# Performance work log

Hardware: AMD Instinct MI355X
Metric: run time of the kernel (lower is better)

Reference implementation:

```python
import jax, jax.numpy as jnp
import numpy as np

NUM_GROUPS = 32
NUM_HEADS = 4
EPS = 1e-5


def setup_inputs() -> dict:
    key = jax.random.key(0)
    ks = jax.random.split(key, 6)
    B, C, H, W = 16, 512, 32, 32
    x = jax.random.normal(ks[0], (B, C, H, W), dtype=jnp.float32)
    gn_w = jax.random.normal(ks[1], (C,), dtype=jnp.float32) * 0.02 + 1.0
    gn_b = jax.random.normal(ks[2], (C,), dtype=jnp.float32) * 0.02
    # 1x1 convs are channel matmuls: store as [out_ch, in_ch]
    w_qkv = jax.random.normal(ks[3], (3 * C, C), dtype=jnp.float32) * (C ** -0.5)
    w_out = jax.random.normal(ks[4], (C, C), dtype=jnp.float32) * (C ** -0.5)
    b_out = jax.random.normal(ks[5], (C,), dtype=jnp.float32) * 0.02
    return {"x": x, "gn_w": gn_w, "gn_b": gn_b, "w_qkv": w_qkv, "w_out": w_out, "b_out": b_out}


def _group_norm(x, w, b):
    B, C, H, W = x.shape
    g = NUM_GROUPS
    xg = x.reshape(B, g, C // g, H, W)
    mean = xg.mean(axis=(2, 3, 4), keepdims=True)
    var = xg.var(axis=(2, 3, 4), keepdims=True)
    xn = ((xg - mean) * jax.lax.rsqrt(var + EPS)).reshape(B, C, H, W)
    return xn * w[None, :, None, None] + b[None, :, None, None]


def reference(x, gn_w, gn_b, w_qkv, w_out, b_out):
    B, C, H, W = x.shape
    h = NUM_HEADS
    d = C // h
    scale = d ** -0.5
    xn = _group_norm(x, gn_w, gn_b)
    # 1x1 conv QKV projection: [3C, C] @ channels
    qkv = jnp.einsum('oc,bchw->bohw', w_qkv, xn)
    q, k, v = jnp.split(qkv, 3, axis=1)
    # [B, h, d, HW]
    q = q.reshape(B, h, d, H * W)
    k = k.reshape(B, h, d, H * W)
    v = v.reshape(B, h, d, H * W)
    scores = jnp.einsum('bhdi,bhdj->bhij', q, k) * scale
    probs = jax.nn.softmax(scores, axis=-1)
    out = jnp.einsum('bhij,bhdj->bhdi', probs, v)
    out = out.reshape(B, C, H, W)
    out = jnp.einsum('oc,bchw->bohw', w_out, out) + b_out[None, :, None, None]
    return out + x
```

## Files before the change

kernel.cpp:

```cpp
#include <hip/hip_runtime.h>
#include <hip/hip_bf16.h>

#define B_    16
#define C_    512
#define HW_   1024
#define G_    32
#define CPG_  16
#define NH_   4
#define D_    128
#define EPS_  1e-5f
#define SCALE_ 0.08838834764831845f
#define SCALE_L2E_ 0.1275174306f

typedef short bf16x8 __attribute__((ext_vector_type(8)));
typedef short bf16x4 __attribute__((ext_vector_type(4)));
typedef float f32x4  __attribute__((ext_vector_type(4)));
typedef float f32x16 __attribute__((ext_vector_type(16)));

typedef __attribute__((address_space(3))) unsigned int lds_u32_t;
typedef const __attribute__((address_space(1))) unsigned int glb_u32_t;

__device__ __forceinline__ bf16x8 ld8(const __hip_bfloat16* p) {
    return *reinterpret_cast<const bf16x8*>(p);
}
__device__ __forceinline__ void gload16(const __hip_bfloat16* g, __hip_bfloat16* l) {
    __builtin_amdgcn_global_load_lds((glb_u32_t*)(const void*)g,
                                     (lds_u32_t*)(void*)l, 16, 0, 0);
}
__device__ __forceinline__ unsigned cvtpk_bf16(float lo, float hi) {
    unsigned r;
    asm("v_cvt_pk_bf16_f32 %0, %1, %2" : "=v"(r) : "v"(lo), "v"(hi));
    return r;
}

__global__ __launch_bounds__(256) void convert_w(
    const float* __restrict__ wqkv, const float* __restrict__ wout,
    __hip_bfloat16* __restrict__ wqkv_bf, __hip_bfloat16* __restrict__ wout_bf) {
    const int i = (blockIdx.x * 256 + threadIdx.x) * 4;
    if (i < 3 * C_ * C_) {
        float4 v = *reinterpret_cast<const float4*>(wqkv + i);
        union { bf16x4 s; __hip_bfloat16 h[4]; } u;
        u.h[0] = __float2bfloat16(v.x); u.h[1] = __float2bfloat16(v.y);
        u.h[2] = __float2bfloat16(v.z); u.h[3] = __float2bfloat16(v.w);
        *reinterpret_cast<bf16x4*>(wqkv_bf + i) = u.s;
    }
    if (i < C_ * C_) {
        float4 v = *reinterpret_cast<const float4*>(wout + i);
        union { bf16x4 s; __hip_bfloat16 h[4]; } u;
        u.h[0] = __float2bfloat16(v.x); u.h[1] = __float2bfloat16(v.y);
        u.h[2] = __float2bfloat16(v.z); u.h[3] = __float2bfloat16(v.w);
        *reinterpret_cast<bf16x4*>(wout_bf + i) = u.s;
    }
}

__global__ __launch_bounds__(256) void gn_kernel(
    const float* __restrict__ x, const float* __restrict__ gnw,
    const float* __restrict__ gnb, __hip_bfloat16* __restrict__ xn_t) {
    const int b = blockIdx.x >> 5;
    const int g = blockIdx.x & 31;
    const float* xp = x + ((size_t)(b * C_ + g * CPG_)) * HW_;

    float s = 0.f, s2 = 0.f;
    const float4* xv = reinterpret_cast<const float4*>(xp);
    #pragma unroll
    for (int t = 0; t < 16; ++t) {
        float4 v = xv[threadIdx.x + t * 256];
        s  += v.x + v.y + v.z + v.w;
        s2 += v.x * v.x + v.y * v.y + v.z * v.z + v.w * v.w;
    }
    #pragma unroll
    for (int off = 32; off > 0; off >>= 1) {
        s  += __shfl_down(s,  off, 64);
        s2 += __shfl_down(s2, off, 64);
    }
    __shared__ float ss[4], ss2[4];
    if ((threadIdx.x & 63) == 0) { ss[threadIdx.x >> 6] = s; ss2[threadIdx.x >> 6] = s2; }
    __syncthreads();
    s = ss[0] + ss[1] + ss[2] + ss[3];
    s2 = ss2[0] + ss2[1] + ss2[2] + ss2[3];
    const float mean = s * (1.f / 16384.f);
    const float inv  = rsqrtf(fmaxf(s2 * (1.f / 16384.f) - mean * mean, 0.f) + EPS_);

    float a[16], bb[16];
    #pragma unroll
    for (int cc = 0; cc < 16; ++cc) {
        float w = gnw[g * CPG_ + cc];
        a[cc] = inv * w;
        bb[cc] = gnb[g * CPG_ + cc] - mean * inv * w;
    }

    for (int hw = threadIdx.x; hw < HW_; hw += 256) {
        union { bf16x8 v; __hip_bfloat16 h[8]; } u0, u1;
        #pragma unroll
        for (int cc = 0; cc < 8; ++cc)
            u0.h[cc] = __float2bfloat16(xp[cc * HW_ + hw] * a[cc] + bb[cc]);
        #pragma unroll
        for (int cc = 8; cc < 16; ++cc)
            u1.h[cc - 8] = __float2bfloat16(xp[cc * HW_ + hw] * a[cc] + bb[cc]);
        __hip_bfloat16* dst = xn_t + ((size_t)(b * HW_ + hw)) * C_ + g * CPG_;
        *reinterpret_cast<bf16x8*>(dst) = u0.v;
        *reinterpret_cast<bf16x8*>(dst + 8) = u1.v;
    }
}

#define PH_(r, s) (((r) * 8 + ((s) ^ ((r) & 7))) * 8)

__global__ __launch_bounds__(256, 2) void qkv_gemm(
    const __hip_bfloat16* __restrict__ W, const __hip_bfloat16* __restrict__ xn_t,
    __hip_bfloat16* __restrict__ q_t, __hip_bfloat16* __restrict__ k_t,
    __hip_bfloat16* __restrict__ v_s) {
    const int id   = blockIdx.x;
    const int virt = (id & 7) * 192 + (id >> 3);
    const int ot   = virt % 12;
    const int rest = virt / 12;
    const int itl  = rest & 7;
    const int b    = rest >> 3;
    const int o0 = ot * 128, i0 = itl * 128;

    const int t = threadIdx.x;
    const int w = t >> 6, lane = t & 63, l16 = lane & 15, lg = lane >> 4;
    const int wr = w >> 1, wc = w & 1;
    const __hip_bfloat16* xb = xn_t + (size_t)b * HW_ * C_;

    __shared__ __align__(16) __hip_bfloat16 Ab[2][128 * 64];
    __shared__ __align__(16) __hip_bfloat16 Bb[2][128 * 64];

    const int r8  = lane >> 3;
    const int ssl = (lane & 7) ^ r8;
    auto issue = [&](int kk, int bi) {
        #pragma unroll
        for (int j = 0; j < 4; ++j) {
            const int row = w * 32 + j * 8 + r8;
            gload16(W  + (size_t)(o0 + row) * C_ + kk + ssl * 8, &Ab[bi][(w * 32 + j * 8) * 64]);
            gload16(xb + (size_t)(i0 + row) * C_ + kk + ssl * 8, &Bb[bi][(w * 32 + j * 8) * 64]);
        }
    };

    f32x4 acc[4][4];
    const f32x4 z = {0.f, 0.f, 0.f, 0.f};
    #pragma unroll
    for (int m = 0; m < 4; ++m)
        #pragma unroll
        for (int n = 0; n < 4; ++n) acc[m][n] = z;

    issue(0, 0);
    for (int ks = 0; ks < 8; ++ks) {
        __syncthreads();
        if (ks < 7) issue((ks + 1) * 64, (ks + 1) & 1);
        const __hip_bfloat16* Ac = Ab[ks & 1];
        const __hip_bfloat16* Bc = Bb[ks & 1];
        #pragma unroll
        for (int kks = 0; kks < 2; ++kks) {
            bf16x8 af[4], bfr[4];
            #pragma unroll
            for (int m = 0; m < 4; ++m)
                af[m] = ld8(&Ac[PH_(wr * 64 + m * 16 + l16, kks * 4 + lg)]);
            #pragma unroll
            for (int n = 0; n < 4; ++n)
                bfr[n] = ld8(&Bc[PH_(wc * 64 + n * 16 + l16, kks * 4 + lg)]);
            if (ot < 8) {
                #pragma unroll
                for (int m = 0; m < 4; ++m)
                    #pragma unroll
                    for (int n = 0; n < 4; ++n)
                        acc[m][n] = __builtin_amdgcn_mfma_f32_16x16x32_bf16(bfr[n], af[m], acc[m][n], 0, 0, 0);
            } else {
                #pragma unroll
                for (int m = 0; m < 4; ++m)
                    #pragma unroll
                    for (int n = 0; n < 4; ++n)
                        acc[m][n] = __builtin_amdgcn_mfma_f32_16x16x32_bf16(af[m], bfr[n], acc[m][n], 0, 0, 0);
            }
        }
    }

    if (ot < 4) {
        const int hd = ot;
        __hip_bfloat16* base = q_t + (size_t)(b * NH_ + hd) * HW_ * D_;
        const int dd = wr * 64 + l16;
        #pragma unroll
        for (int m = 0; m < 4; ++m)
            #pragma unroll
            for (int n = 0; n < 4; ++n)
                #pragma unroll
                for (int r = 0; r < 4; ++r) {
                    const int i = i0 + wc * 64 + n * 16 + lg * 4 + r;
                    base[(size_t)i * D_ + dd + m * 16] = __float2bfloat16(acc[m][n][r] * SCALE_L2E_);
                }
    } else if (ot < 8) {
        const int hd = ot - 4;
        __hip_bfloat16* base = k_t + (size_t)(b * NH_ + hd) * HW_ * D_;
        const int dd = wr * 64 + l16;
        #pragma unroll
        for (int m = 0; m < 4; ++m)
            #pragma unroll
            for (int n = 0; n < 4; ++n)
                #pragma unroll
                for (int r = 0; r < 4; ++r) {
                    const int i = i0 + wc * 64 + n * 16 + lg * 4 + r;
                    base[(size_t)i * D_ + dd + m * 16] = __float2bfloat16(acc[m][n][r]);
                }
    } else {
        const int hd = ot - 8;
        __hip_bfloat16* base = v_s + (size_t)(b * NH_ + hd) * D_ * HW_;
        #pragma unroll
        for (int m = 0; m < 4; ++m)
            #pragma unroll
            for (int r = 0; r < 4; ++r) {
                const int dd = wr * 64 + m * 16 + lg * 4 + r;
                #pragma unroll
                for (int n = 0; n < 4; ++n) {
                    const int i = i0 + wc * 64 + n * 16 + l16;
                    base[(size_t)dd * HW_ + i] = __float2bfloat16(acc[m][n][r]);
                }
            }
    }
}

__global__ __launch_bounds__(256, 2) void attn_kernel(
    const __hip_bfloat16* __restrict__ q_t, const __hip_bfloat16* __restrict__ k_t,
    const __hip_bfloat16* __restrict__ v_s, __hip_bfloat16* __restrict__ at) {
    const int id  = blockIdx.x;
    const int xcd = id & 7;
    const int q8  = id >> 3;
    const int hb  = xcd * 8 + (q8 >> 3);
    const int it  = q8 & 7;
    const int h   = hb & 3;
    const int b   = hb >> 2;

    const int t = threadIdx.x;
    const int w  = t >> 6;
    const int lane = t & 63;
    const int l32 = lane & 31;
    const int hi  = lane >> 5;
    const size_t bh = (size_t)b * NH_ + h;
    const __hip_bfloat16* qp = q_t + bh * HW_ * D_;
    const __hip_bfloat16* kp = k_t + bh * HW_ * D_;
    const __hip_bfloat16* vp = v_s + bh * D_ * HW_;
    const int i0 = it * 128 + w * 32;

    __shared__ __align__(16) char smem[2][16384];

    #define KPHYS(row, c) (((row) * 16 + ((c) ^ ((row) & 7))) * 8)
    #define VPHYS(row, c) (((row) * 4  + ((c) ^ (((row) >> 1) & 3))) * 8)

    const int kri = lane >> 4, ksl = lane & 15;
    const int vri = lane >> 2, vsl = lane & 3;
    auto issue = [&](int j0, int bi) {
        __hip_bfloat16* kb = (__hip_bfloat16*)(smem[bi]);
        __hip_bfloat16* vb = (__hip_bfloat16*)(smem[bi] + 8192);
        #pragma unroll
        for (int i = 0; i < 2; ++i) {
            const int kr = w * 8 + i * 4 + kri;
            gload16(kp + (size_t)(j0 + kr) * D_ + ((ksl ^ (kr & 7)) * 8),
                    kb + (w * 8 + i * 4) * 128);
            const int vr = w * 32 + i * 16 + vri;
            gload16(vp + (size_t)vr * HW_ + j0 + ((vsl ^ ((vr >> 1) & 3)) * 8),
                    vb + (w * 32 + i * 16) * 32);
        }
    };

    bf16x8 aq[8];
    #pragma unroll
    for (int ds = 0; ds < 8; ++ds)
        aq[ds] = ld8(qp + (size_t)(i0 + l32) * D_ + ds * 16 + hi * 8);

    f32x16 accO[4];
    #pragma unroll
    for (int d = 0; d < 4; ++d)
        #pragma unroll
        for (int e = 0; e < 16; ++e) accO[d][e] = 0.f;
    float m_run = -INFINITY;
    float l_run = 0.f;

    issue(0, 0);

    for (int jb = 0; jb < 32; ++jb) {
        __syncthreads();
        if (jb < 31) issue((jb + 1) * 32, (jb + 1) & 1);
        const __hip_bfloat16* kb = (const __hip_bfloat16*)(smem[jb & 1]);
        const __hip_bfloat16* vb = (const __hip_bfloat16*)(smem[jb & 1] + 8192);

        f32x16 st;
        #pragma unroll
        for (int e = 0; e < 16; ++e) st[e] = 0.f;
        #pragma unroll
        for (int ds = 0; ds < 8; ++ds) {
            bf16x8 kf = ld8(&kb[KPHYS(l32, ds * 2 + hi)]);
            st = __builtin_amdgcn_mfma_f32_32x32x16_bf16(kf, aq[ds], st, 0, 0, 0);
        }

        float mx = fmaxf(st[0], st[1]);
        #pragma unroll
        for (int r = 2; r < 16; ++r) mx = fmaxf(mx, st[r]);
        mx = fmaxf(mx, __shfl_xor(mx, 32, 64));

        if (__any(mx > m_run + 8.f)) {
            float mnew = fmaxf(m_run, mx);
            float alpha = exp2f(m_run - mnew);
            m_run = mnew;
            l_run *= alpha;
            #pragma unroll
            for (int d = 0; d < 4; ++d)
                #pragma unroll
                for (int e = 0; e < 16; ++e) accO[d][e] *= alpha;
        }

        float p[16];
        float sum = 0.f;
        #pragma unroll
        for (int r = 0; r < 16; ++r) { p[r] = exp2f(st[r] - m_run); sum += p[r]; }
        sum += __shfl_xor(sum, 32, 64);
        l_run += sum;

        #define PV_STEP(KS) do {                                                \
            const int g0 = (KS) * 2;                                            \
            unsigned a0 = cvtpk_bf16(p[g0 * 4 + 0], p[g0 * 4 + 1]);             \
            unsigned a1 = cvtpk_bf16(p[g0 * 4 + 2], p[g0 * 4 + 3]);             \
            unsigned b0 = cvtpk_bf16(p[g0 * 4 + 4], p[g0 * 4 + 5]);             \
            unsigned b1 = cvtpk_bf16(p[g0 * 4 + 6], p[g0 * 4 + 7]);             \
            asm volatile("v_permlane32_swap_b32 %0, %1" : "+v"(a0), "+v"(b0));  \
            asm volatile("v_permlane32_swap_b32 %0, %1" : "+v"(a1), "+v"(b1));  \
            union { unsigned u[4]; bf16x8 v; } pf;                              \
            pf.u[0] = a0; pf.u[1] = a1; pf.u[2] = b0; pf.u[3] = b1;             \
            _Pragma("unroll")                                                   \
            for (int dt = 0; dt < 4; ++dt) {                                    \
                bf16x8 vf = ld8(&vb[VPHYS(dt * 32 + l32, (KS) * 2 + hi)]);      \
                accO[dt] = __builtin_amdgcn_mfma_f32_32x32x16_bf16(              \
                    vf, pf.v, accO[dt], 0, 0, 0);                               \
            }                                                                   \
        } while (0)
        PV_STEP(0);
        PV_STEP(1);
        #undef PV_STEP
    }

    const float linv = 1.f / l_run;
    __hip_bfloat16* ob = at + ((size_t)b * HW_ + i0) * C_ + h * D_;
    __syncthreads();
    #pragma unroll
    for (int pass = 0; pass < 2; ++pass) {
        if ((w >> 1) == pass) {
            __hip_bfloat16* Ep = (__hip_bfloat16*)smem + (w & 1) * (32 * 132);
            #pragma unroll
            for (int dt = 0; dt < 4; ++dt)
                #pragma unroll
                for (int r = 0; r < 16; ++r) {
                    const int d = dt * 32 + (r & 3) + 4 * hi + 8 * (r >> 2);
                    Ep[l32 * 132 + d] = __float2bfloat16(accO[dt][r] * linv);
                }
            #pragma unroll
            for (int rr = 0; rr < 8; ++rr) {
                const int row = rr * 4 + (lane >> 4);
                const int col = (lane & 15) * 8;
                bf16x8 vv = ld8(&Ep[row * 132 + col]);
                *reinterpret_cast<bf16x8*>(ob + (size_t)row * C_ + col) = vv;
            }
        }
        __syncthreads();
    }
    #undef KPHYS
    #undef VPHYS
}

__global__ __launch_bounds__(256, 2) void out_gemm(
    const __hip_bfloat16* __restrict__ W, const __hip_bfloat16* __restrict__ at,
    const float* __restrict__ b_out, const float* __restrict__ x,
    float* __restrict__ out) {
    const int id   = blockIdx.x;
    const int virt = (id & 7) * 64 + (id >> 3);
    const int ot   = virt & 3;
    const int rest = virt >> 2;
    const int itl  = rest & 7;
    const int b    = rest >> 3;
    const int o0 = ot * 128, i0 = itl * 128;

    const int t = threadIdx.x;
    const int w = t >> 6, lane = t & 63, l16 = lane & 15, lg = lane >> 4;
    const int wr = w >> 1, wc = w & 1;
    const __hip_bfloat16* ab = at + (size_t)b * HW_ * C_;

    __shared__ __align__(16) __hip_bfloat16 Ab[2][128 * 64];
    __shared__ __align__(16) __hip_bfloat16 Bb[2][128 * 64];

    const int r8  = lane >> 3;
    const int ssl = (lane & 7) ^ r8;
    auto issue = [&](int kk, int bi) {
        #pragma unroll
        for (int j = 0; j < 4; ++j) {
            const int row = w * 32 + j * 8 + r8;
            gload16(W  + (size_t)(o0 + row) * C_ + kk + ssl * 8, &Ab[bi][(w * 32 + j * 8) * 64]);
            gload16(ab + (size_t)(i0 + row) * C_ + kk + ssl * 8, &Bb[bi][(w * 32 + j * 8) * 64]);
        }
    };

    f32x4 acc[4][4];
    const f32x4 z = {0.f, 0.f, 0.f, 0.f};
    #pragma unroll
    for (int m = 0; m < 4; ++m)
        #pragma unroll
        for (int n = 0; n < 4; ++n) acc[m][n] = z;

    issue(0, 0);
    for (int ks = 0; ks < 8; ++ks) {
        __syncthreads();
        if (ks < 7) issue((ks + 1) * 64, (ks + 1) & 1);
        const __hip_bfloat16* Ac = Ab[ks & 1];
        const __hip_bfloat16* Bc = Bb[ks & 1];
        #pragma unroll
        for (int kks = 0; kks < 2; ++kks) {
            bf16x8 af[4], bfr[4];
            #pragma unroll
            for (int m = 0; m < 4; ++m)
                af[m] = ld8(&Ac[PH_(wr * 64 + m * 16 + l16, kks * 4 + lg)]);
            #pragma unroll
            for (int n = 0; n < 4; ++n)
                bfr[n] = ld8(&Bc[PH_(wc * 64 + n * 16 + l16, kks * 4 + lg)]);
            #pragma unroll
            for (int m = 0; m < 4; ++m)
                #pragma unroll
                for (int n = 0; n < 4; ++n)
                    acc[m][n] = __builtin_amdgcn_mfma_f32_16x16x32_bf16(af[m], bfr[n], acc[m][n], 0, 0, 0);
        }
    }

    #pragma unroll
    for (int m = 0; m < 4; ++m)
        #pragma unroll
        for (int r = 0; r < 4; ++r) {
            const int o = o0 + wr * 64 + m * 16 + lg * 4 + r;
            const float bo = b_out[o];
            #pragma unroll
            for (int n = 0; n < 4; ++n) {
                const int i = i0 + wc * 64 + n * 16 + l16;
                const size_t idx = ((size_t)(b * C_ + o)) * HW_ + i;
                out[idx] = acc[m][n][r] + bo + x[idx];
            }
        }
}

extern "C" void kernel_launch(void* const* d_in, const int* in_sizes, int n_in,
                              void* d_out, int out_size, void* d_ws, size_t ws_size,
                              hipStream_t stream) {
    (void)in_sizes; (void)n_in; (void)out_size; (void)ws_size;
    const float* x     = (const float*)d_in[0];
    const float* gn_w  = (const float*)d_in[1];
    const float* gn_b  = (const float*)d_in[2];
    const float* w_qkv = (const float*)d_in[3];
    const float* w_out = (const float*)d_in[4];
    const float* b_out = (const float*)d_in[5];
    float* out = (float*)d_out;

    char* ws = (char*)d_ws;
    size_t off = 0;
    auto alloc = [&](size_t bytes) { void* p = ws + off; off += (bytes + 255) & ~255ULL; return p; };
    __hip_bfloat16* wqkv_bf = (__hip_bfloat16*)alloc((size_t)3 * C_ * C_ * 2);
    __hip_bfloat16* wout_bf = (__hip_bfloat16*)alloc((size_t)C_ * C_ * 2);
    __hip_bfloat16* xn_t    = (__hip_bfloat16*)alloc((size_t)B_ * HW_ * C_ * 2);
    __hip_bfloat16* q_t     = (__hip_bfloat16*)alloc((size_t)B_ * HW_ * C_ * 2);
    __hip_bfloat16* k_t     = (__hip_bfloat16*)alloc((size_t)B_ * HW_ * C_ * 2);
    __hip_bfloat16* v_s     = (__hip_bfloat16*)alloc((size_t)B_ * HW_ * C_ * 2);
    __hip_bfloat16* at      = xn_t;

    convert_w<<<768, 256, 0, stream>>>(w_qkv, w_out, wqkv_bf, wout_bf);
    gn_kernel<<<512, 256, 0, stream>>>(x, gn_w, gn_b, xn_t);
    qkv_gemm<<<1536, 256, 0, stream>>>(wqkv_bf, xn_t, q_t, k_t, v_s);
    attn_kernel<<<512, 256, 0, stream>>>(q_t, k_t, v_s, at);
    out_gemm<<<512, 256, 0, stream>>>(wout_bf, at, b_out, x, out);
}
```

Measured before the change: 127.2 us.

## Split attention KV range across two warp groups and merge softmax partials

The attention block grows from 256 to 512 threads. Two groups of four waves each process half of the key/value sequence for the same 128 query rows, using separate double-buffered LDS tiles. At the end the partial max, sum and output accumulators are merged through shared memory with rescaling before the normalized output is written. This raises wave-level parallelism per CU and halves each wave's serial KV loop, at the cost of extra LDS use, several added barriers, and a merge epilogue.

```diff
diff --git a/kernel.cpp b/kernel.cpp
--- a/kernel.cpp
+++ b/kernel.cpp
@@ -217,7 +217,7 @@
     }
 }
 
-__global__ __launch_bounds__(256, 2) void attn_kernel(
+__global__ __launch_bounds__(512, 2) void attn_kernel(
     const __hip_bfloat16* __restrict__ q_t, const __hip_bfloat16* __restrict__ k_t,
     const __hip_bfloat16* __restrict__ v_s, __hip_bfloat16* __restrict__ at) {
     const int id  = blockIdx.x;
@@ -230,6 +230,8 @@
 
     const int t = threadIdx.x;
     const int w  = t >> 6;
+    const int qt = w & 3;
+    const int g  = w >> 2;
     const int lane = t & 63;
     const int l32 = lane & 31;
     const int hi  = lane >> 5;
@@ -237,26 +239,27 @@
     const __hip_bfloat16* qp = q_t + bh * HW_ * D_;
     const __hip_bfloat16* kp = k_t + bh * HW_ * D_;
     const __hip_bfloat16* vp = v_s + bh * D_ * HW_;
-    const int i0 = it * 128 + w * 32;
-
-    __shared__ __align__(16) char smem[2][16384];
+    const int i0 = it * 128 + qt * 32;
+
+    __shared__ __align__(16) char smem[2][2][16384];
 
     #define KPHYS(row, c) (((row) * 16 + ((c) ^ ((row) & 7))) * 8)
     #define VPHYS(row, c) (((row) * 4  + ((c) ^ (((row) >> 1) & 3))) * 8)
 
     const int kri = lane >> 4, ksl = lane & 15;
     const int vri = lane >> 2, vsl = lane & 3;
-    auto issue = [&](int j0, int bi) {
-        __hip_bfloat16* kb = (__hip_bfloat16*)(smem[bi]);
-        __hip_bfloat16* vb = (__hip_bfloat16*)(smem[bi] + 8192);
+    auto issue = [&](int jb, int bi) {
+        const int j0 = g * 512 + jb * 32;
+        __hip_bfloat16* kb = (__hip_bfloat16*)(smem[g][bi]);
+        __hip_bfloat16* vb = (__hip_bfloat16*)(smem[g][bi] + 8192);
         #pragma unroll
         for (int i = 0; i < 2; ++i) {
-            const int kr = w * 8 + i * 4 + kri;
+            const int kr = qt * 8 + i * 4 + kri;
             gload16(kp + (size_t)(j0 + kr) * D_ + ((ksl ^ (kr & 7)) * 8),
-                    kb + (w * 8 + i * 4) * 128);
-            const int vr = w * 32 + i * 16 + vri;
+                    kb + (qt * 8 + i * 4) * 128);
+            const int vr = qt * 32 + i * 16 + vri;
             gload16(vp + (size_t)vr * HW_ + j0 + ((vsl ^ ((vr >> 1) & 3)) * 8),
-                    vb + (w * 32 + i * 16) * 32);
+                    vb + (qt * 32 + i * 16) * 32);
         }
     };
 
@@ -275,11 +278,11 @@
 
     issue(0, 0);
 
-    for (int jb = 0; jb < 32; ++jb) {
+    for (int jb = 0; jb < 16; ++jb) {
         __syncthreads();
-        if (jb < 31) issue((jb + 1) * 32, (jb + 1) & 1);
-        const __hip_bfloat16* kb = (const __hip_bfloat16*)(smem[jb & 1]);
-        const __hip_bfloat16* vb = (const __hip_bfloat16*)(smem[jb & 1] + 8192);
+        if (jb < 15) issue(jb + 1, (jb + 1) & 1);
+        const __hip_bfloat16* kb = (const __hip_bfloat16*)(smem[g][jb & 1]);
+        const __hip_bfloat16* vb = (const __hip_bfloat16*)(smem[g][jb & 1] + 8192);
 
         f32x16 st;
         #pragma unroll
@@ -335,29 +338,72 @@
         #undef PV_STEP
     }
 
-    const float linv = 1.f / l_run;
-    __hip_bfloat16* ob = at + ((size_t)b * HW_ + i0) * C_ + h * D_;
+    float* fsm = (float*)smem;
+    float* ml  = fsm;
+    float* ch  = fsm + 512;
+    float f0 = 1.f, f1 = 0.f;
     __syncthreads();
-    #pragma unroll
-    for (int pass = 0; pass < 2; ++pass) {
-        if ((w >> 1) == pass) {
-            __hip_bfloat16* Ep = (__hip_bfloat16*)smem + (w & 1) * (32 * 132);
-            #pragma unroll
-            for (int dt = 0; dt < 4; ++dt)
-                #pragma unroll
-                for (int r = 0; r < 16; ++r) {
-                    const int d = dt * 32 + (r & 3) + 4 * hi + 8 * (r >> 2);
-                    Ep[l32 * 132 + d] = __float2bfloat16(accO[dt][r] * linv);
-                }
-            #pragma unroll
-            for (int rr = 0; rr < 8; ++rr) {
-                const int row = rr * 4 + (lane >> 4);
-                const int col = (lane & 15) * 8;
-                bf16x8 vv = ld8(&Ep[row * 132 + col]);
-                *reinterpret_cast<bf16x8*>(ob + (size_t)row * C_ + col) = vv;
+    if (g == 1) {
+        ml[(qt * 2 + 0) * 64 + lane] = m_run;
+        ml[(qt * 2 + 1) * 64 + lane] = l_run;
+        float* c = ch + (qt * 64 + lane) * 33;
+        #pragma unroll
+        for (int d = 0; d < 2; ++d)
+            #pragma unroll
+            for (int e = 0; e < 16; ++e) c[d * 16 + e] = accO[d][e];
+    }
+    __syncthreads();
+    if (g == 0) {
+        const float m1 = ml[(qt * 2 + 0) * 64 + lane];
+        const float l1 = ml[(qt * 2 + 1) * 64 + lane];
+        const float mn = fmaxf(m_run, m1);
+        f0 = exp2f(m_run - mn); f1 = exp2f(m1 - mn);
+        l_run = l_run * f0 + l1 * f1;
+        m_run = mn;
+        const float* c = ch + (qt * 64 + lane) * 33;
+        #pragma unroll
+        for (int d = 0; d < 2; ++d)
+            #pragma unroll
+            for (int e = 0; e < 16; ++e)
+                accO[d][e] = accO[d][e] * f0 + c[d * 16 + e] * f1;
+    }
+    __syncthreads();
+    if (g == 1) {
+        float* c = ch + (qt * 64 + lane) * 33;
+        #pragma unroll
+        for (int d = 0; d < 2; ++d)
+            #pragma unroll
+            for (int e = 0; e < 16; ++e) c[d * 16 + e] = accO[2 + d][e];
+    }
+    __syncthreads();
+    if (g == 0) {
+        const float* c = ch + (qt * 64 + lane) * 33;
+        #pragma unroll
+        for (int d = 0; d < 2; ++d)
+            #pragma unroll
+            for (int e = 0; e < 16; ++e)
+                accO[2 + d][e] = accO[2 + d][e] * f0 + c[d * 16 + e] * f1;
+    }
+    __syncthreads();
+
+    if (g == 0) {
+        const float linv = 1.f / l_run;
+        __hip_bfloat16* Ep = (__hip_bfloat16*)smem + qt * (32 * 132);
+        #pragma unroll
+        for (int dt = 0; dt < 4; ++dt)
+            #pragma unroll
+            for (int r = 0; r < 16; ++r) {
+                const int d = dt * 32 + (r & 3) + 4 * hi + 8 * (r >> 2);
+                Ep[l32 * 132 + d] = __float2bfloat16(accO[dt][r] * linv);
             }
-        }
-        __syncthreads();
+        __hip_bfloat16* ob = at + ((size_t)b * HW_ + i0) * C_ + h * D_;
+        #pragma unroll
+        for (int rr = 0; rr < 8; ++rr) {
+            const int row = rr * 4 + (lane >> 4);
+            const int col = (lane & 15) * 8;
+            bf16x8 vv = ld8(&Ep[row * 132 + col]);
+            *reinterpret_cast<bf16x8*>(ob + (size_t)row * C_ + col) = vv;
+        }
     }
     #undef KPHYS
     #undef VPHYS
@@ -465,6 +511,6 @@
     convert_w<<<768, 256, 0, stream>>>(w_qkv, w_out, wqkv_bf, wout_bf);
     gn_kernel<<<512, 256, 0, stream>>>(x, gn_w, gn_b, xn_t);
     qkv_gemm<<<1536, 256, 0, stream>>>(wqkv_bf, xn_t, q_t, k_t, v_s);
-    attn_kernel<<<512, 256, 0, stream>>>(q_t, k_t, v_s, at);
+    attn_kernel<<<512, 512, 0, stream>>>(q_t, k_t, v_s, at);
     out_gemm<<<512, 256, 0, stream>>>(wout_bf, at, b_out, x, out);
 }
```

New measurement: 133.5 us. 1.05x slower.
